# Performance work log

Hardware: AMD Instinct MI355X
Metric: run time of the kernel (lower is better)

The kernel has to match this reference:

```python
import jax, jax.numpy as jnp
import numpy as np

N_NODES = 50000
N_EDGES = 800000
IN_DIM = 128
EDGE_DIM = 64
OUT_DIM = 128


def setup_inputs() -> dict:
    key = jax.random.key(0)
    ks = jax.random.split(key, 9)
    nfeat = jax.random.normal(ks[0], (N_NODES, IN_DIM), dtype=jnp.float32)
    efeat = jax.random.normal(ks[1], (N_EDGES, EDGE_DIM), dtype=jnp.float32)
    src = jax.random.randint(ks[2], (N_EDGES,), 0, N_NODES, dtype=jnp.int32)
    dst = jax.random.randint(ks[3], (N_EDGES,), 0, N_NODES, dtype=jnp.int32)
    # learned params (Kaiming-ish scaling)
    W_edge = jax.random.normal(ks[4], (EDGE_DIM, OUT_DIM), dtype=jnp.float32) / np.float32(np.sqrt(EDGE_DIM))
    W_ne = jax.random.normal(ks[5], (IN_DIM + OUT_DIM, OUT_DIM), dtype=jnp.float32) / np.float32(np.sqrt(IN_DIM + OUT_DIM))
    b_ne = jnp.zeros((OUT_DIM,), dtype=jnp.float32)
    W_self = jax.random.normal(ks[6], (IN_DIM, OUT_DIM), dtype=jnp.float32) / np.float32(np.sqrt(IN_DIM))
    b_self = jnp.zeros((OUT_DIM,), dtype=jnp.float32)
    return {"nfeat": nfeat, "efeat": efeat, "src": src, "dst": dst,
            "W_edge": W_edge, "W_ne": W_ne, "b_ne": b_ne,
            "W_self": W_self, "b_self": b_self}


def reference(nfeat, efeat, src, dst, W_edge, W_ne, b_ne, W_self, b_self):
    # per-edge message: relu(Linear(concat(src_h, edge_map(efeat))))
    eh = efeat @ W_edge                      # [E, OUT]
    src_h = nfeat[src]                        # [E, IN]  (gather)
    # split-matmul form of concat([src_h, eh]) @ W_ne (identical math, no concat buffer)
    m = jax.nn.relu(src_h @ W_ne[:IN_DIM] + eh @ W_ne[IN_DIM:] + b_ne)  # [E, OUT]
    # segment-mean scatter by destination node (dgl.function.mean -> 0 for isolated nodes)
    summ = jax.ops.segment_sum(m, dst, num_segments=N_NODES)             # [N, OUT]
    cnt = jax.ops.segment_sum(jnp.ones((m.shape[0], 1), m.dtype), dst, num_segments=N_NODES)
    neigh = summ / jnp.maximum(cnt, 1.0)
    # self transform
    out = neigh + nfeat @ W_self + b_self
    return out
```

## Files before the change

### kernel.cpp

```cpp
#include <hip/hip_runtime.h>

#define N_NODES 50000
#define N_EDGES 800000
#define IN_DIM  128
#define EDGE_DIM 64
#define OUT_DIM 128
#define NTILES  (N_EDGES / 128)
#define NODE_TILES ((N_NODES + 127) / 128)
#define W2_BLOCKS 32
#define ZERO_BLOCKS 196

typedef __attribute__((ext_vector_type(8))) short bf16x8;
typedef __attribute__((ext_vector_type(4))) float f32x4;
typedef unsigned short u16;

__device__ __forceinline__ u16 f2bf(float f) {
    union { float f; unsigned u; } x; x.f = f;
    unsigned r = x.u + 0x7FFFu + ((x.u >> 16) & 1u);
    return (u16)(r >> 16);
}
__device__ __forceinline__ float bf2f(u16 h) {
    union { unsigned u; float f; } x; x.u = ((unsigned)h) << 16;
    return x.f;
}
__device__ __forceinline__ bf16x8 pack8(const float* v) {
    bf16x8 r;
#pragma unroll
    for (int i = 0; i < 8; ++i) r[i] = (short)f2bf(v[i]);
    return r;
}

__global__ __launch_bounds__(256, 1) void prep_kernel(
    const float* __restrict__ nfeat, const float* __restrict__ W_ne,
    const float* __restrict__ W_self, const float* __restrict__ b_self,
    const float* __restrict__ W_edge,
    u16* __restrict__ H1, u16* __restrict__ HS,
    float* __restrict__ W2fT, int* __restrict__ cnts) {

    __shared__ __align__(16) char Nb[128 * 128 * 2];

    const int bid = blockIdx.x;
    const int tid = threadIdx.x;

    if (bid >= NODE_TILES) {
        if (bid < NODE_TILES + W2_BLOCKS) {
            const int idx = (bid - NODE_TILES) * 256 + tid;
            const int c = idx >> 7;
            const int o = idx & 127;
            float acc = 0.0f;
            for (int i = 0; i < OUT_DIM; ++i)
                acc += W_edge[c * OUT_DIM + i] * W_ne[(IN_DIM + i) * OUT_DIM + o];
            W2fT[o * EDGE_DIM + c] = acc;
        } else {
            const int i = (bid - NODE_TILES - W2_BLOCKS) * 256 + tid;
            if (i < N_NODES) cnts[i] = 0;
        }
        return;
    }

    const int w    = tid >> 6;
    const int l    = tid & 63;
    const int lrow = l & 15;
    const int lq   = l >> 4;

    const bool isSelf = (w >= 2);
    const float* W = isSelf ? W_self : W_ne;
    const int colw = (w & 1) * 64;
    u16* Y = isSelf ? HS : H1;

    bf16x8 Wf[4][4];
#pragma unroll
    for (int mt = 0; mt < 4; ++mt) {
        const int c = colw + mt * 16 + lrow;
#pragma unroll
        for (int kk = 0; kk < 4; ++kk) {
            float tmp[8];
#pragma unroll
            for (int t = 0; t < 8; ++t) tmp[t] = W[(kk * 32 + lq * 8 + t) * 128 + c];
            Wf[mt][kk] = pack8(tmp);
        }
    }
    float4 bias4[4];
#pragma unroll
    for (int mt = 0; mt < 4; ++mt) {
        if (isSelf) bias4[mt] = *(const float4*)(b_self + colw + mt * 16 + lq * 4);
        else { bias4[mt].x = 0.f; bias4[mt].y = 0.f; bias4[mt].z = 0.f; bias4[mt].w = 0.f; }
    }

    const int srow = tid >> 1;
    const int skc  = (tid & 1) * 8;
    const int r0 = bid * 128;
    {
        const int gr = min(r0 + srow, N_NODES - 1);
        const float4* np = (const float4*)(nfeat + (size_t)gr * 128 + skc * 8);
        const int swz = (srow & 7);
#pragma unroll
        for (int j = 0; j < 8; ++j) {
            float4 x = np[2 * j], y = np[2 * j + 1];
            float tmp[8] = {x.x, x.y, x.z, x.w, y.x, y.y, y.z, y.w};
            bf16x8 f = pack8(tmp);
            const int kc = skc + j;
            *(bf16x8*)(Nb + srow * 256 + (((kc) ^ swz) * 16)) = f;
        }
    }
    __syncthreads();

    f32x4 acc[4][8];
#pragma unroll
    for (int mt = 0; mt < 4; ++mt)
#pragma unroll
        for (int nt = 0; nt < 8; ++nt) {
            acc[mt][nt][0] = bias4[mt].x; acc[mt][nt][1] = bias4[mt].y;
            acc[mt][nt][2] = bias4[mt].z; acc[mt][nt][3] = bias4[mt].w;
        }
#pragma unroll
    for (int nt = 0; nt < 8; ++nt) {
        const int r = nt * 16 + lrow;
        const int swz = (r & 7);
        bf16x8 Be[4];
#pragma unroll
        for (int kk = 0; kk < 4; ++kk)
            Be[kk] = *(const bf16x8*)(Nb + r * 256 + (((kk * 4 + lq) ^ swz) * 16));
#pragma unroll
        for (int mt = 0; mt < 4; ++mt)
#pragma unroll
            for (int kk = 0; kk < 4; ++kk)
                acc[mt][nt] = __builtin_amdgcn_mfma_f32_16x16x32_bf16(Wf[mt][kk], Be[kk], acc[mt][nt], 0, 0, 0);
    }

#pragma unroll
    for (int nt = 0; nt < 8; ++nt) {
        const int n = r0 + nt * 16 + lrow;
        if (n < N_NODES) {
#pragma unroll
            for (int mt = 0; mt < 4; ++mt) {
                const int c0 = colw + mt * 16 + lq * 4;
                ushort4 o;
                o.x = f2bf(acc[mt][nt][0]); o.y = f2bf(acc[mt][nt][1]);
                o.z = f2bf(acc[mt][nt][2]); o.w = f2bf(acc[mt][nt][3]);
                *(ushort4*)(Y + (size_t)n * 128 + c0) = o;
            }
        }
    }
}

__global__ void count_rank_kernel(const int* __restrict__ dst,
                                  int* __restrict__ counts, int* __restrict__ rank) {
    const int e = blockIdx.x * blockDim.x + threadIdx.x;
    if (e < N_EDGES) rank[e] = atomicAdd(&counts[dst[e]], 1);
}

#define SCAN_T 1024
#define SCAN_CHUNK 49
__global__ void scan_kernel(const int* __restrict__ counts, int* __restrict__ off) {
    __shared__ int part[SCAN_T];
    const int t = threadIdx.x;
    const int base = t * SCAN_CHUNK;
    int s = 0;
    for (int k = 0; k < SCAN_CHUNK; ++k) {
        const int i = base + k;
        if (i < N_NODES) s += counts[i];
    }
    part[t] = s;
    __syncthreads();
    for (int d = 1; d < SCAN_T; d <<= 1) {
        int v = (t >= d) ? part[t - d] : 0;
        __syncthreads();
        part[t] += v;
        __syncthreads();
    }
    int excl = part[t] - s;
    for (int k = 0; k < SCAN_CHUNK; ++k) {
        const int i = base + k;
        if (i < N_NODES) { off[i] = excl; excl += counts[i]; }
    }
    if (t == SCAN_T - 1) off[N_NODES] = excl;
}

__global__ __launch_bounds__(256, 3) void edge_gemm_scatter_kernel(
    const float* __restrict__ efeat, const int* __restrict__ src,
    const int* __restrict__ dst, const int* __restrict__ rank,
    const int* __restrict__ offs, const float* __restrict__ W2fT,
    const float* __restrict__ b_ne, const u16* __restrict__ H1,
    u16* __restrict__ mbuf) {

    __shared__ __align__(16) char Ab[128 * 64 * 2];
    __shared__ int sS[128];
    __shared__ int sT[128];

    const int tid  = threadIdx.x;
    const int w    = tid >> 6;
    const int l    = tid & 63;
    const int lrow = l & 15;
    const int lq   = l >> 4;

    bf16x8 Wf[2][2];
    float4 bias4[2];
#pragma unroll
    for (int mt = 0; mt < 2; ++mt) {
        const int c = w * 32 + mt * 16 + lrow;
#pragma unroll
        for (int kk = 0; kk < 2; ++kk) {
            const float* wp = W2fT + c * 64 + kk * 32 + lq * 8;
            float tmp[8];
#pragma unroll
            for (int j = 0; j < 8; ++j) tmp[j] = wp[j];
            Wf[mt][kk] = pack8(tmp);
        }
        bias4[mt] = *(const float4*)(b_ne + w * 32 + mt * 16 + lq * 4);
    }

    const int srow = tid >> 1;
    const int skh  = (tid & 1) * 32;

    for (int tile = blockIdx.x; tile < NTILES; tile += gridDim.x) {
        const int e0 = tile * 128;

        if (tid < 128) {
            const int e = e0 + tid;
            sS[tid] = src[e];
            sT[tid] = offs[dst[e]] + rank[e];
        }
        {
            const float4* ep = (const float4*)(efeat + (size_t)(e0 + srow) * 64 + skh);
            const int swz = (srow & 7) << 4;
#pragma unroll
            for (int j = 0; j < 4; ++j) {
                float4 x = ep[2 * j], y = ep[2 * j + 1];
                float tmp[8] = {x.x, x.y, x.z, x.w, y.x, y.y, y.z, y.w};
                bf16x8 f = pack8(tmp);
                *(bf16x8*)(Ab + ((srow * 128 + skh * 2 + j * 16) ^ swz)) = f;
            }
        }
        __syncthreads();

        f32x4 acc[2][8];
#pragma unroll
        for (int mt = 0; mt < 2; ++mt)
#pragma unroll
            for (int nt = 0; nt < 8; ++nt) {
                acc[mt][nt][0] = bias4[mt].x; acc[mt][nt][1] = bias4[mt].y;
                acc[mt][nt][2] = bias4[mt].z; acc[mt][nt][3] = bias4[mt].w;
            }
#pragma unroll
        for (int nt = 0; nt < 8; ++nt) {
            const int r = nt * 16 + lrow;
            const int swz = (r & 7) << 4;
            bf16x8 Be0 = *(const bf16x8*)(Ab + ((r * 128 + lq * 16) ^ swz));
            bf16x8 Be1 = *(const bf16x8*)(Ab + ((r * 128 + 64 + lq * 16) ^ swz));
#pragma unroll
            for (int mt = 0; mt < 2; ++mt) {
                acc[mt][nt] = __builtin_amdgcn_mfma_f32_16x16x32_bf16(Wf[mt][0], Be0, acc[mt][nt], 0, 0, 0);
                acc[mt][nt] = __builtin_amdgcn_mfma_f32_16x16x32_bf16(Wf[mt][1], Be1, acc[mt][nt], 0, 0, 0);
            }
        }

#pragma unroll
        for (int nt = 0; nt < 8; ++nt) {
            const int e  = nt * 16 + lrow;
            const int sn = sS[e];
            const int st = sT[e];
#pragma unroll
            for (int mt = 0; mt < 2; ++mt) {
                const int c0 = w * 32 + mt * 16 + lq * 4;
                ushort4 h4 = *(const ushort4*)(H1 + (size_t)sn * 128 + c0);
                ushort4 o;
                o.x = f2bf(fmaxf(acc[mt][nt][0] + bf2f(h4.x), 0.0f));
                o.y = f2bf(fmaxf(acc[mt][nt][1] + bf2f(h4.y), 0.0f));
                o.z = f2bf(fmaxf(acc[mt][nt][2] + bf2f(h4.z), 0.0f));
                o.w = f2bf(fmaxf(acc[mt][nt][3] + bf2f(h4.w), 0.0f));
                *(ushort4*)(mbuf + (size_t)st * 128 + c0) = o;
            }
        }
        __syncthreads();
    }
}

__global__ __launch_bounds__(256, 4) void reduce_kernel(
    const int* __restrict__ off, const u16* __restrict__ mbuf,
    const u16* __restrict__ HS, float* __restrict__ out) {
    const int n = (blockIdx.x * blockDim.x + threadIdx.x) >> 6;
    if (n >= N_NODES) return;
    const int l  = threadIdx.x & 63;
    const int cs = l & 15;
    const int rg = l >> 4;
    const int s0 = off[n], s1 = off[n + 1];

    float facc[8];
#pragma unroll
    for (int i = 0; i < 8; ++i) facc[i] = 0.0f;
    for (int s = s0 + rg; s < s1; s += 4) {
        bf16x8 v = *(const bf16x8*)(mbuf + (size_t)s * 128 + cs * 8);
#pragma unroll
        for (int i = 0; i < 8; ++i) facc[i] += bf2f((u16)v[i]);
    }
#pragma unroll
    for (int i = 0; i < 8; ++i) {
        facc[i] += __shfl_xor(facc[i], 16, 64);
        facc[i] += __shfl_xor(facc[i], 32, 64);
    }
    if (rg == 0) {
        const int c = s1 - s0;
        const float inv = (c > 0) ? 1.0f / (float)c : 0.0f;
        bf16x8 hs = *(const bf16x8*)(HS + (size_t)n * 128 + cs * 8);
        float4 o0, o1;
        o0.x = facc[0] * inv + bf2f((u16)hs[0]);
        o0.y = facc[1] * inv + bf2f((u16)hs[1]);
        o0.z = facc[2] * inv + bf2f((u16)hs[2]);
        o0.w = facc[3] * inv + bf2f((u16)hs[3]);
        o1.x = facc[4] * inv + bf2f((u16)hs[4]);
        o1.y = facc[5] * inv + bf2f((u16)hs[5]);
        o1.z = facc[6] * inv + bf2f((u16)hs[6]);
        o1.w = facc[7] * inv + bf2f((u16)hs[7]);
        float* op = out + (size_t)n * 128 + cs * 8;
        *(float4*)op = o0;
        *(float4*)(op + 4) = o1;
    }
}

extern "C" void kernel_launch(void* const* d_in, const int* in_sizes, int n_in,
                              void* d_out, int out_size, void* d_ws, size_t ws_size,
                              hipStream_t stream) {
    const float* nfeat  = (const float*)d_in[0];
    const float* efeat  = (const float*)d_in[1];
    const int*   src    = (const int*)d_in[2];
    const int*   dst    = (const int*)d_in[3];
    const float* W_edge = (const float*)d_in[4];
    const float* W_ne   = (const float*)d_in[5];
    const float* b_ne   = (const float*)d_in[6];
    const float* W_self = (const float*)d_in[7];
    const float* b_self = (const float*)d_in[8];

    float* out = (float*)d_out;
    char* ws = (char*)d_ws;

    const size_t OFF_W2   = 0;
    const size_t OFF_CNT  = 32768;
    const size_t OFF_OFFS = 232960;
    const size_t OFF_RANK = 433152;
    const size_t OFF_H1   = 3633152;
    const size_t OFF_HS   = 16433152;
    const size_t OFF_M    = 29233152;

    float* W2fT = (float*)(ws + OFF_W2);
    int*   cnts = (int*)(ws + OFF_CNT);
    int*   offs = (int*)(ws + OFF_OFFS);
    int*   rank = (int*)(ws + OFF_RANK);
    u16*   H1   = (u16*)(ws + OFF_H1);
    u16*   HS   = (u16*)(ws + OFF_HS);
    u16*   mbuf = (u16*)(ws + OFF_M);

    prep_kernel<<<NODE_TILES + W2_BLOCKS + ZERO_BLOCKS, 256, 0, stream>>>(
        nfeat, W_ne, W_self, b_self, W_edge, H1, HS, W2fT, cnts);
    count_rank_kernel<<<(N_EDGES + 255) / 256, 256, 0, stream>>>(dst, cnts, rank);
    scan_kernel<<<1, SCAN_T, 0, stream>>>(cnts, offs);
    edge_gemm_scatter_kernel<<<2048, 256, 0, stream>>>(
        efeat, src, dst, rank, offs, W2fT, b_ne, H1, mbuf);
    reduce_kernel<<<(N_NODES * 64 + 255) / 256, 256, 0, stream>>>(offs, mbuf, HS, out);
}
```

Measured before the change: 355.6 us.

## Fuse edge GEMM and segment-mean into per-node kernel using sorted edge ids

Replaces the edge-tile GEMM that wrote a bf16 per-edge message buffer, and the separate reduce kernel, with a CSR-style approach. A scatter kernel builds destination-sorted edge-id and source arrays. A per-node kernel (one wave per node) gathers efeat and H1 rows, runs the small MFMA GEMM in 16-edge passes, and accumulates the ReLU'd messages directly into the node mean before adding the self term. The edge counting is folded into prep_kernel behind a memset. This removes the write and re-read of the 800K x 128 message buffer. In exchange, efeat reads become random gathers and degree imbalance plus padded partial passes waste MFMA work.

```diff
diff --git a/kernel.cpp b/kernel.cpp
--- a/kernel.cpp
+++ b/kernel.cpp
@@ -5,12 +5,12 @@
 #define IN_DIM  128
 #define EDGE_DIM 64
 #define OUT_DIM 128
-#define NTILES  (N_EDGES / 128)
 #define NODE_TILES ((N_NODES + 127) / 128)
 #define W2_BLOCKS 32
-#define ZERO_BLOCKS 196
+#define CNT_BLOCKS ((N_EDGES + 255) / 256)
 
 typedef __attribute__((ext_vector_type(8))) short bf16x8;
+typedef __attribute__((ext_vector_type(4))) short bf16x4;
 typedef __attribute__((ext_vector_type(4))) float f32x4;
 typedef unsigned short u16;
 
@@ -33,9 +33,9 @@
 __global__ __launch_bounds__(256, 1) void prep_kernel(
     const float* __restrict__ nfeat, const float* __restrict__ W_ne,
     const float* __restrict__ W_self, const float* __restrict__ b_self,
-    const float* __restrict__ W_edge,
+    const float* __restrict__ W_edge, const int* __restrict__ dst,
     u16* __restrict__ H1, u16* __restrict__ HS,
-    float* __restrict__ W2fT, int* __restrict__ cnts) {
+    float* __restrict__ W2fT, int* __restrict__ cnts, int* __restrict__ rank) {
 
     __shared__ __align__(16) char Nb[128 * 128 * 2];
 
@@ -52,8 +52,8 @@
                 acc += W_edge[c * OUT_DIM + i] * W_ne[(IN_DIM + i) * OUT_DIM + o];
             W2fT[o * EDGE_DIM + c] = acc;
         } else {
-            const int i = (bid - NODE_TILES - W2_BLOCKS) * 256 + tid;
-            if (i < N_NODES) cnts[i] = 0;
+            const int e = (bid - NODE_TILES - W2_BLOCKS) * 256 + tid;
+            if (e < N_EDGES) rank[e] = atomicAdd(&cnts[dst[e]], 1);
         }
         return;
     }
@@ -142,12 +142,6 @@
             }
         }
     }
-}
-
-__global__ void count_rank_kernel(const int* __restrict__ dst,
-                                  int* __restrict__ counts, int* __restrict__ rank) {
-    const int e = blockIdx.x * blockDim.x + threadIdx.x;
-    if (e < N_EDGES) rank[e] = atomicAdd(&counts[dst[e]], 1);
 }
 
 #define SCAN_T 1024
@@ -177,145 +171,132 @@
     if (t == SCAN_T - 1) off[N_NODES] = excl;
 }
 
-__global__ __launch_bounds__(256, 3) void edge_gemm_scatter_kernel(
-    const float* __restrict__ efeat, const int* __restrict__ src,
-    const int* __restrict__ dst, const int* __restrict__ rank,
-    const int* __restrict__ offs, const float* __restrict__ W2fT,
-    const float* __restrict__ b_ne, const u16* __restrict__ H1,
-    u16* __restrict__ mbuf) {
-
-    __shared__ __align__(16) char Ab[128 * 64 * 2];
-    __shared__ int sS[128];
-    __shared__ int sT[128];
+__global__ void scatter_kernel(const int* __restrict__ dst, const int* __restrict__ src,
+                               const int* __restrict__ rank, const int* __restrict__ off,
+                               int* __restrict__ eidS, int* __restrict__ srcS) {
+    const int e = blockIdx.x * blockDim.x + threadIdx.x;
+    if (e < N_EDGES) {
+        const int slot = off[dst[e]] + rank[e];
+        eidS[slot] = e;
+        srcS[slot] = src[e];
+    }
+}
+
+__global__ __launch_bounds__(256, 2) void fused_node_kernel(
+    const float* __restrict__ efeat, const int* __restrict__ eidS,
+    const int* __restrict__ srcS, const int* __restrict__ offs,
+    const float* __restrict__ W2fT, const float* __restrict__ b_ne,
+    const u16* __restrict__ H1, const u16* __restrict__ HS,
+    float* __restrict__ out) {
+
+    __shared__ __align__(16) char LA[4][16 * 128];
+    __shared__ __align__(16) char LH[4][16 * 256];
 
     const int tid  = threadIdx.x;
     const int w    = tid >> 6;
     const int l    = tid & 63;
     const int lrow = l & 15;
     const int lq   = l >> 4;
-
-    bf16x8 Wf[2][2];
-    float4 bias4[2];
-#pragma unroll
-    for (int mt = 0; mt < 2; ++mt) {
-        const int c = w * 32 + mt * 16 + lrow;
+    const int gi   = lrow;
+
+    char* A = LA[w];
+    char* H = LH[w];
+
+    bf16x8 Bf[8][2];
+    float bias[8];
+#pragma unroll
+    for (int nt = 0; nt < 8; ++nt) {
+        bias[nt] = b_ne[nt * 16 + lrow];
 #pragma unroll
         for (int kk = 0; kk < 2; ++kk) {
-            const float* wp = W2fT + c * 64 + kk * 32 + lq * 8;
+            const float* wp = W2fT + (nt * 16 + lrow) * 64 + kk * 32 + lq * 8;
             float tmp[8];
 #pragma unroll
             for (int j = 0; j < 8; ++j) tmp[j] = wp[j];
-            Wf[mt][kk] = pack8(tmp);
-        }
-        bias4[mt] = *(const float4*)(b_ne + w * 32 + mt * 16 + lq * 4);
-    }
-
-    const int srow = tid >> 1;
-    const int skh  = (tid & 1) * 32;
-
-    for (int tile = blockIdx.x; tile < NTILES; tile += gridDim.x) {
-        const int e0 = tile * 128;
-
-        if (tid < 128) {
-            const int e = e0 + tid;
-            sS[tid] = src[e];
-            sT[tid] = offs[dst[e]] + rank[e];
-        }
-        {
-            const float4* ep = (const float4*)(efeat + (size_t)(e0 + srow) * 64 + skh);
-            const int swz = (srow & 7) << 4;
-#pragma unroll
-            for (int j = 0; j < 4; ++j) {
-                float4 x = ep[2 * j], y = ep[2 * j + 1];
-                float tmp[8] = {x.x, x.y, x.z, x.w, y.x, y.y, y.z, y.w};
-                bf16x8 f = pack8(tmp);
-                *(bf16x8*)(Ab + ((srow * 128 + skh * 2 + j * 16) ^ swz)) = f;
+            Bf[nt][kk] = pack8(tmp);
+        }
+    }
+
+    const int n = blockIdx.x * 4 + w;
+    if (n >= N_NODES) return;
+    const int s0 = offs[n], s1 = offs[n + 1];
+    const int deg = s1 - s0;
+
+    float nodeSum[8];
+#pragma unroll
+    for (int nt = 0; nt < 8; ++nt) nodeSum[nt] = 0.0f;
+
+    const int npass = (deg + 15) >> 4;
+    for (int p = 0; p < npass; ++p) {
+        const int base = s0 + p * 16;
+
+#pragma unroll
+        for (int it = 0; it < 4; ++it) {
+            const int r = lq * 4 + it;
+            int slot = base + r;
+            if (slot >= s1) slot = s1 - 1;
+            const int e  = eidS[slot];
+            const int sc = srcS[slot];
+
+            float4 f4 = *(const float4*)(efeat + (size_t)e * 64 + gi * 4);
+            ushort4 a4;
+            a4.x = f2bf(f4.x); a4.y = f2bf(f4.y); a4.z = f2bf(f4.z); a4.w = f2bf(f4.w);
+            *(ushort4*)(A + r * 128 + ((gi * 8) ^ ((r & 7) << 4))) = a4;
+
+            bf16x8 hv = *(const bf16x8*)(H1 + (size_t)sc * 128 + gi * 8);
+            const int hs8 = (r & 7) << 3;
+            *(bf16x4*)(H + r * 256 + ((gi * 16) ^ hs8))     = *(((const bf16x4*)&hv));
+            *(bf16x4*)(H + r * 256 + ((gi * 16 + 8) ^ hs8)) = *(((const bf16x4*)&hv) + 1);
+        }
+
+        bf16x8 Af[2];
+#pragma unroll
+        for (int kk = 0; kk < 2; ++kk)
+            Af[kk] = *(const bf16x8*)(A + lrow * 128 + ((kk * 64 + lq * 16) ^ ((lrow & 7) << 4)));
+
+        f32x4 acc[8];
+#pragma unroll
+        for (int nt = 0; nt < 8; ++nt) {
+            acc[nt][0] = bias[nt]; acc[nt][1] = bias[nt];
+            acc[nt][2] = bias[nt]; acc[nt][3] = bias[nt];
+            acc[nt] = __builtin_amdgcn_mfma_f32_16x16x32_bf16(Af[0], Bf[nt][0], acc[nt], 0, 0, 0);
+            acc[nt] = __builtin_amdgcn_mfma_f32_16x16x32_bf16(Af[1], Bf[nt][1], acc[nt], 0, 0, 0);
+        }
+
+        const int remain = deg - p * 16;
+#pragma unroll
+        for (int j = 0; j < 4; ++j) {
+            const int row = lq * 4 + j;
+            const bool valid = row < remain;
+            const int hs8 = (row & 7) << 3;
+#pragma unroll
+            for (int nt = 0; nt < 8; ++nt) {
+                const int col = nt * 16 + lrow;
+                const u16 h = *(const u16*)(H + row * 256 + ((col * 2) ^ hs8));
+                float v = fmaxf(acc[nt][j] + bf2f(h), 0.0f);
+                if (valid) nodeSum[nt] += v;
             }
         }
-        __syncthreads();
-
-        f32x4 acc[2][8];
-#pragma unroll
-        for (int mt = 0; mt < 2; ++mt)
-#pragma unroll
-            for (int nt = 0; nt < 8; ++nt) {
-                acc[mt][nt][0] = bias4[mt].x; acc[mt][nt][1] = bias4[mt].y;
-                acc[mt][nt][2] = bias4[mt].z; acc[mt][nt][3] = bias4[mt].w;
-            }
-#pragma unroll
-        for (int nt = 0; nt < 8; ++nt) {
-            const int r = nt * 16 + lrow;
-            const int swz = (r & 7) << 4;
-            bf16x8 Be0 = *(const bf16x8*)(Ab + ((r * 128 + lq * 16) ^ swz));
-            bf16x8 Be1 = *(const bf16x8*)(Ab + ((r * 128 + 64 + lq * 16) ^ swz));
-#pragma unroll
-            for (int mt = 0; mt < 2; ++mt) {
-                acc[mt][nt] = __builtin_amdgcn_mfma_f32_16x16x32_bf16(Wf[mt][0], Be0, acc[mt][nt], 0, 0, 0);
-                acc[mt][nt] = __builtin_amdgcn_mfma_f32_16x16x32_bf16(Wf[mt][1], Be1, acc[mt][nt], 0, 0, 0);
-            }
-        }
-
-#pragma unroll
-        for (int nt = 0; nt < 8; ++nt) {
-            const int e  = nt * 16 + lrow;
-            const int sn = sS[e];
-            const int st = sT[e];
-#pragma unroll
-            for (int mt = 0; mt < 2; ++mt) {
-                const int c0 = w * 32 + mt * 16 + lq * 4;
-                ushort4 h4 = *(const ushort4*)(H1 + (size_t)sn * 128 + c0);
-                ushort4 o;
-                o.x = f2bf(fmaxf(acc[mt][nt][0] + bf2f(h4.x), 0.0f));
-                o.y = f2bf(fmaxf(acc[mt][nt][1] + bf2f(h4.y), 0.0f));
-                o.z = f2bf(fmaxf(acc[mt][nt][2] + bf2f(h4.z), 0.0f));
-                o.w = f2bf(fmaxf(acc[mt][nt][3] + bf2f(h4.w), 0.0f));
-                *(ushort4*)(mbuf + (size_t)st * 128 + c0) = o;
-            }
-        }
-        __syncthreads();
-    }
-}
-
-__global__ __launch_bounds__(256, 4) void reduce_kernel(
-    const int* __restrict__ off, const u16* __restrict__ mbuf,
-    const u16* __restrict__ HS, float* __restrict__ out) {
-    const int n = (blockIdx.x * blockDim.x + threadIdx.x) >> 6;
-    if (n >= N_NODES) return;
-    const int l  = threadIdx.x & 63;
-    const int cs = l & 15;
-    const int rg = l >> 4;
-    const int s0 = off[n], s1 = off[n + 1];
-
-    float facc[8];
-#pragma unroll
-    for (int i = 0; i < 8; ++i) facc[i] = 0.0f;
-    for (int s = s0 + rg; s < s1; s += 4) {
-        bf16x8 v = *(const bf16x8*)(mbuf + (size_t)s * 128 + cs * 8);
-#pragma unroll
-        for (int i = 0; i < 8; ++i) facc[i] += bf2f((u16)v[i]);
-    }
-#pragma unroll
-    for (int i = 0; i < 8; ++i) {
-        facc[i] += __shfl_xor(facc[i], 16, 64);
-        facc[i] += __shfl_xor(facc[i], 32, 64);
-    }
-    if (rg == 0) {
-        const int c = s1 - s0;
-        const float inv = (c > 0) ? 1.0f / (float)c : 0.0f;
-        bf16x8 hs = *(const bf16x8*)(HS + (size_t)n * 128 + cs * 8);
-        float4 o0, o1;
-        o0.x = facc[0] * inv + bf2f((u16)hs[0]);
-        o0.y = facc[1] * inv + bf2f((u16)hs[1]);
-        o0.z = facc[2] * inv + bf2f((u16)hs[2]);
-        o0.w = facc[3] * inv + bf2f((u16)hs[3]);
-        o1.x = facc[4] * inv + bf2f((u16)hs[4]);
-        o1.y = facc[5] * inv + bf2f((u16)hs[5]);
-        o1.z = facc[6] * inv + bf2f((u16)hs[6]);
-        o1.w = facc[7] * inv + bf2f((u16)hs[7]);
-        float* op = out + (size_t)n * 128 + cs * 8;
-        *(float4*)op = o0;
-        *(float4*)(op + 4) = o1;
-    }
+    }
+
+#pragma unroll
+    for (int nt = 0; nt < 8; ++nt) {
+        nodeSum[nt] += __shfl_xor(nodeSum[nt], 16, 64);
+        nodeSum[nt] += __shfl_xor(nodeSum[nt], 32, 64);
+    }
+
+    const float inv = (deg > 0) ? 1.0f / (float)deg : 0.0f;
+    if (lq == 0) {
+#pragma unroll
+        for (int nt = 0; nt < 8; ++nt)
+            *(float*)(A + (nt * 16 + lrow) * 4) = nodeSum[nt] * inv;
+    }
+    float2 r2 = *(const float2*)(A + l * 8);
+    const unsigned hs2 = *(const unsigned*)(HS + (size_t)n * 128 + l * 2);
+    float2 o2;
+    o2.x = r2.x + bf2f((u16)(hs2 & 0xffff));
+    o2.y = r2.y + bf2f((u16)(hs2 >> 16));
+    *(float2*)(out + (size_t)n * 128 + l * 2) = o2;
 }
 
 extern "C" void kernel_launch(void* const* d_in, const int* in_sizes, int n_in,
@@ -337,24 +318,26 @@
     const size_t OFF_W2   = 0;
     const size_t OFF_CNT  = 32768;
     const size_t OFF_OFFS = 232960;
-    const size_t OFF_RANK = 433152;
-    const size_t OFF_H1   = 3633152;
-    const size_t OFF_HS   = 16433152;
-    const size_t OFF_M    = 29233152;
+    const size_t OFF_RANK = 433408;
+    const size_t OFF_EID  = 3633408;
+    const size_t OFF_SRCS = 6833408;
+    const size_t OFF_H1   = 10033408;
+    const size_t OFF_HS   = 22833408;
 
     float* W2fT = (float*)(ws + OFF_W2);
     int*   cnts = (int*)(ws + OFF_CNT);
     int*   offs = (int*)(ws + OFF_OFFS);
     int*   rank = (int*)(ws + OFF_RANK);
+    int*   eidS = (int*)(ws + OFF_EID);
+    int*   srcS = (int*)(ws + OFF_SRCS);
     u16*   H1   = (u16*)(ws + OFF_H1);
     u16*   HS   = (u16*)(ws + OFF_HS);
-    u16*   mbuf = (u16*)(ws + OFF_M);
-
-    prep_kernel<<<NODE_TILES + W2_BLOCKS + ZERO_BLOCKS, 256, 0, stream>>>(
-        nfeat, W_ne, W_self, b_self, W_edge, H1, HS, W2fT, cnts);
-    count_rank_kernel<<<(N_EDGES + 255) / 256, 256, 0, stream>>>(dst, cnts, rank);
+
+    hipMemsetAsync(cnts, 0, N_NODES * sizeof(int), stream);
+    prep_kernel<<<NODE_TILES + W2_BLOCKS + CNT_BLOCKS, 256, 0, stream>>>(
+        nfeat, W_ne, W_self, b_self, W_edge, dst, H1, HS, W2fT, cnts, rank);
     scan_kernel<<<1, SCAN_T, 0, stream>>>(cnts, offs);
-    edge_gemm_scatter_kernel<<<2048, 256, 0, stream>>>(
-        efeat, src, dst, rank, offs, W2fT, b_ne, H1, mbuf);
-    reduce_kernel<<<(N_NODES * 64 + 255) / 256, 256, 0, stream>>>(offs, mbuf, HS, out);
-}
+    scatter_kernel<<<(N_EDGES + 255) / 256, 256, 0, stream>>>(dst, src, rank, offs, eidS, srcS);
+    fused_node_kernel<<<(N_NODES + 3) / 4, 256, 0, stream>>>(
+        efeat, eidS, srcS, offs, W2fT, b_ne, H1, HS, out);
+}
```

New measurement: 445.2 us. 25.2% more time.
